# Kernel tuning notes

Measured on AMD Instinct MI355X. Metric: run time of the kernel, lower is better.

## Reference

```python
import jax, jax.numpy as jnp
import numpy as np

EPS = 1e-5

def _face_normals(v, vi):
    # v: [B,V,3], vi: [F,3] -> [B,F,3]
    pts = v[:, vi]                                  # [B,F,3,3]
    n = jnp.cross(pts[:, :, 1] - pts[:, :, 0], pts[:, :, 2] - pts[:, :, 0])
    norm = jnp.linalg.norm(n, axis=-1, keepdims=True)
    return n / jnp.where(norm < EPS, 1.0, norm)

def _vert_normals(v, vi):
    fn = _face_normals(v, vi)                       # [B,F,3]
    fn_rep = jnp.repeat(fn, 3, axis=1)              # [B,3F,3] (one copy per face vertex)
    vn = jnp.zeros_like(v).at[:, vi.reshape(-1)].add(fn_rep)
    norm = jnp.linalg.norm(vn, axis=-1, keepdims=True)
    return vn / jnp.where(norm < EPS, 1.0, norm)

def _values_to_uv(values, index_image, bary_image):
    # values: [B,V,C]; index_image/bary_image: [U,U,3] -> [B,C,U,U]
    mask = jnp.all(index_image != -1, axis=-1)      # [U,U]
    idx = jnp.clip(index_image, 0, values.shape[1] - 1)
    vals = values[:, idx]                           # [B,U,U,3,C]
    uv = jnp.einsum('buvkc,uvk->bcuv', vals, bary_image.astype(values.dtype))
    return uv * mask[None, None].astype(values.dtype)

def _grid_sample_bilinear(img, gx, gy):
    # img: [B,C,H,W]; gx,gy: [N] in [-1,1]; align_corners=False, zero padding
    B, C, H, W = img.shape
    ix = ((gx + 1.0) * W - 1.0) * 0.5
    iy = ((gy + 1.0) * H - 1.0) * 0.5
    x0 = jnp.floor(ix); y0 = jnp.floor(iy)
    x1 = x0 + 1.0;      y1 = y0 + 1.0
    wx1 = ix - x0; wx0 = 1.0 - wx1
    wy1 = iy - y0; wy0 = 1.0 - wy1
    def gather(xi, yi):
        valid = (xi >= 0) & (xi < W) & (yi >= 0) & (yi < H)
        xc = jnp.clip(xi, 0, W - 1).astype(jnp.int32)
        yc = jnp.clip(yi, 0, H - 1).astype(jnp.int32)
        return img[:, :, yc, xc] * valid.astype(img.dtype)  # [B,C,N]
    return (gather(x0, y0) * (wx0 * wy0) + gather(x1, y0) * (wx1 * wy0)
          + gather(x0, y1) * (wx0 * wy1) + gather(x1, y1) * (wx1 * wy1))

def _sample_uv(values_uv, uv_coords, v2uv):
    g = uv_coords * 2.0 - 1.0                       # [T,2]
    vals = _grid_sample_bilinear(values_uv, g[:, 0], g[:, 1])  # [B,C,T]
    vals = jnp.transpose(vals, (0, 2, 1))           # [B,T,C]
    return vals[:, v2uv].mean(axis=2)               # [B,V,C]

def setup_inputs() -> dict:
    key = jax.random.key(0)
    ks = jax.random.split(key, 6)
    B, V, Fc, U, T, K = 8, 100000, 200000, 1024, 110000, 2
    verts = jax.random.normal(ks[0], (B, V, 3), jnp.float32)
    vi = jax.random.randint(ks[1], (Fc, 3), 0, V, dtype=jnp.int32)
    index_image = jax.random.randint(ks[2], (U, U, 3), 0, V, dtype=jnp.int32)
    bary_image = jax.random.uniform(ks[3], (U, U, 3), jnp.float32)
    vt = jax.random.uniform(ks[4], (T, 2), jnp.float32)
    v2uv = jax.random.randint(ks[5], (V, K), 0, T, dtype=jnp.int32)
    return {"verts": verts, "bary_image": bary_image, "vt": vt,
            "vi": vi, "index_image": index_image, "v2uv": v2uv}

def reference(verts, bary_image, vt, vi, index_image, v2uv):
    vn = _vert_normals(verts, vi)                   # [B,V,3]
    uv = _values_to_uv(vn, index_image, bary_image) # [B,3,U,U]
    return _sample_uv(uv, vt, v2uv)                 # [B,V,3]
```

## Files before the change

### kernel.cpp

```cpp
#include <hip/hip_runtime.h>

#define EPS 1e-5f

constexpr int B = 8;
constexpr int V = 100000;
constexpr int F = 200000;
constexpr int U = 1024;
constexpr int T = 110000;
constexpr int CAP = 24;

constexpr int NBUK = (V + 127) / 128;
constexpr int N4   = (3 * F) / 4;
constexpr int EB   = (N4 + 255) / 256;
constexpr int TRB  = (V + 255) / 256;
constexpr int FNB  = (F * 8 + 255) / 256;
constexpr int CPB  = (T + 255) / 256;

__global__ void k1_pre(const float* __restrict__ verts,
                       float4* __restrict__ vertsT,
                       const int* __restrict__ vi,
                       int* __restrict__ hist) {
    __shared__ int lh[NBUK];
    int blk = blockIdx.x;
    if (blk < TRB) {
        int v = blk * 256 + threadIdx.x;
        if (v >= V) return;
        float4 row[8];
#pragma unroll
        for (int b = 0; b < 8; ++b) {
            const float* p = verts + (size_t)b * V * 3 + (size_t)v * 3;
            row[b] = make_float4(p[0], p[1], p[2], 0.0f);
        }
        float4* dst = vertsT + (size_t)v * 8;
#pragma unroll
        for (int b = 0; b < 8; ++b) dst[b] = row[b];
    } else {
        int k = blk - TRB;
        for (int i = threadIdx.x; i < NBUK; i += 256) lh[i] = 0;
        __syncthreads();
        int m4 = k * 256 + threadIdx.x;
        if (m4 < N4) {
            int4 e = ((const int4*)vi)[m4];
            atomicAdd(&lh[e.x >> 7], 1);
            atomicAdd(&lh[e.y >> 7], 1);
            atomicAdd(&lh[e.z >> 7], 1);
            atomicAdd(&lh[e.w >> 7], 1);
        }
        __syncthreads();
        for (int b = threadIdx.x; b < NBUK; b += 256) hist[k * NBUK + b] = lh[b];
    }
}

__global__ void k2_fused(const int* __restrict__ vi,
                         const float4* __restrict__ vertsT,
                         float4* __restrict__ fn,
                         const int* __restrict__ index_image,
                         const float* __restrict__ bary_image,
                         const float* __restrict__ vt,
                         int4* __restrict__ cI,
                         float4* __restrict__ cW,
                         int* __restrict__ hist,
                         int* __restrict__ tot) {
    int blk = blockIdx.x;

    if (blk < FNB) {
        int id = blk * 256 + threadIdx.x;
        if (id >= F * 8) return;
        int f = id >> 3;
        int b = id & 7;

        int i0 = vi[f * 3 + 0];
        int i1 = vi[f * 3 + 1];
        int i2 = vi[f * 3 + 2];

        float4 p0 = vertsT[(size_t)i0 * 8 + b];
        float4 p1 = vertsT[(size_t)i1 * 8 + b];
        float4 p2 = vertsT[(size_t)i2 * 8 + b];

        float e1x = p1.x - p0.x, e1y = p1.y - p0.y, e1z = p1.z - p0.z;
        float e2x = p2.x - p0.x, e2y = p2.y - p0.y, e2z = p2.z - p0.z;

        float nx = e1y * e2z - e1z * e2y;
        float ny = e1z * e2x - e1x * e2z;
        float nz = e1x * e2y - e1y * e2x;

        float norm = sqrtf(nx * nx + ny * ny + nz * nz);
        float inv = (norm < EPS) ? 1.0f : (1.0f / norm);
        fn[id] = make_float4(nx * inv, ny * inv, nz * inv, 0.0f);
        return;
    }

    if (blk < FNB + CPB) {
        int t = (blk - FNB) * 256 + threadIdx.x;
        if (t >= T) return;

        float gx = vt[t * 2 + 0];
        float gy = vt[t * 2 + 1];
        float ix = gx * (float)U - 0.5f;
        float iy = gy * (float)U - 0.5f;

        float x0f = floorf(ix);
        float y0f = floorf(iy);
        int x0 = (int)x0f;
        int y0 = (int)y0f;
        float wx1 = ix - x0f, wx0 = 1.0f - wx1;
        float wy1 = iy - y0f, wy0 = 1.0f - wy1;

#pragma unroll
        for (int c = 0; c < 4; ++c) {
            int cy = c >> 1, cx = c & 1;
            int y = y0 + cy;
            int x = x0 + cx;
            int4 ci = make_int4(0, 0, 0, 0);
            float4 cw = make_float4(0.0f, 0.0f, 0.0f, 0.0f);
            if (x >= 0 && x < U && y >= 0 && y < U) {
                float w = (cy ? wy1 : wy0) * (cx ? wx1 : wx0);
                int pix = y * U + x;
                int i0 = index_image[pix * 3 + 0];
                int i1 = index_image[pix * 3 + 1];
                int i2 = index_image[pix * 3 + 2];
                float m = (i0 != -1 && i1 != -1 && i2 != -1) ? 1.0f : 0.0f;
                float wm = w * m;
                ci.x = min(max(i0, 0), V - 1);
                ci.y = min(max(i1, 0), V - 1);
                ci.z = min(max(i2, 0), V - 1);
                cw.x = wm * bary_image[pix * 3 + 0];
                cw.y = wm * bary_image[pix * 3 + 1];
                cw.z = wm * bary_image[pix * 3 + 2];
            }
            cI[t * 4 + c] = ci;
            cW[t * 4 + c] = cw;
        }
        return;
    }

    {
        __shared__ int part[256];
        int b = blk - FNB - CPB;
        int th = threadIdx.x;
        int k0 = th * 3;
        int c0 = (k0     < EB) ? hist[(k0    ) * NBUK + b] : 0;
        int c1 = (k0 + 1 < EB) ? hist[(k0 + 1) * NBUK + b] : 0;
        int c2 = (k0 + 2 < EB) ? hist[(k0 + 2) * NBUK + b] : 0;
        int local = c0 + c1 + c2;
        part[th] = local;
        __syncthreads();
        for (int off = 1; off < 256; off <<= 1) {
            int x = (th >= off) ? part[th - off] : 0;
            __syncthreads();
            part[th] += x;
            __syncthreads();
        }
        int excl = part[th] - local;
        if (th == 255) tot[b] = part[255];
        if (k0     < EB) hist[(k0    ) * NBUK + b] = excl;
        if (k0 + 1 < EB) hist[(k0 + 1) * NBUK + b] = excl + c0;
        if (k0 + 2 < EB) hist[(k0 + 2) * NBUK + b] = excl + c0 + c1;
    }
}

__global__ void k3_base(const int* __restrict__ tot, int* __restrict__ base) {
    __shared__ int s[1024];
    int t = threadIdx.x;
    int c = (t < NBUK) ? tot[t] : 0;
    s[t] = c;
    __syncthreads();
    for (int off = 1; off < 1024; off <<= 1) {
        int x = (t >= off) ? s[t - off] : 0;
        __syncthreads();
        s[t] += x;
        __syncthreads();
    }
    if (t <= NBUK) base[t] = s[t] - c;
}

__global__ void k4_scatter(const int* __restrict__ vi,
                           const int* __restrict__ off,
                           const int* __restrict__ base,
                           int* __restrict__ pairs) {
    __shared__ int lh[NBUK];
    int k = blockIdx.x;
    for (int i = threadIdx.x; i < NBUK; i += 256) lh[i] = 0;
    __syncthreads();
    int m4 = k * 256 + threadIdx.x;
    if (m4 >= N4) return;
    int4 e = ((const int4*)vi)[m4];
    int be = m4 * 4;
    int vv[4] = {e.x, e.y, e.z, e.w};
#pragma unroll
    for (int j = 0; j < 4; ++j) {
        int v = vv[j];
        int b = v >> 7;
        int r = atomicAdd(&lh[b], 1);
        int pos = base[b] + off[k * NBUK + b] + r;
        pairs[pos] = ((v & 127) << 18) | ((be + j) / 3);
    }
}

__global__ __launch_bounds__(512) void k5_gather(
        const int* __restrict__ pairs,
        const int* __restrict__ base,
        const float4* __restrict__ fn,
        float4* __restrict__ vn) {
    __shared__ int cnt[128];
    __shared__ int rows[128 * CAP];
    int b = blockIdx.x;
    int tid = threadIdx.x;
    if (tid < 128) cnt[tid] = 0;
    __syncthreads();

    int start = base[b], end = base[b + 1];
    for (int i = start + tid; i < end; i += 512) {
        int pk = pairs[i];
        int vl = pk >> 18;
        int f = pk & 0x3FFFF;
        int pos = atomicAdd(&cnt[vl], 1);
        if (pos < CAP) rows[vl * CAP + pos] = f;
    }
    __syncthreads();

    int v0 = b << 7;
    for (int id = tid; id < 128 * 8; id += 512) {
        int vl = id >> 3, b8 = id & 7;
        int v = v0 + vl;
        if (v >= V) continue;
        int deg = min(cnt[vl], CAP);
        float ax = 0.0f, ay = 0.0f, az = 0.0f;
        for (int j = 0; j < deg; ++j) {
            float4 n = fn[(size_t)rows[vl * CAP + j] * 8 + b8];
            ax += n.x; ay += n.y; az += n.z;
        }
        float nn = sqrtf(ax * ax + ay * ay + az * az);
        float inv = (nn < EPS) ? 1.0f : (1.0f / nn);
        vn[(size_t)v * 8 + b8] = make_float4(ax * inv, ay * inv, az * inv, 0.0f);
    }
}

__global__ void sample_points(const float4* __restrict__ vn,
                              const int4* __restrict__ cI,
                              const float4* __restrict__ cW,
                              float4* __restrict__ vals) {
    int id = blockIdx.x * blockDim.x + threadIdx.x;
    if (id >= T * 8) return;
    int t = id >> 3;
    int b = id & 7;

    float ax = 0.0f, ay = 0.0f, az = 0.0f;
#pragma unroll
    for (int c = 0; c < 4; ++c) {
        int4 ci = cI[t * 4 + c];
        float4 cw = cW[t * 4 + c];
        float4 q0 = vn[(size_t)ci.x * 8 + b];
        float4 q1 = vn[(size_t)ci.y * 8 + b];
        float4 q2 = vn[(size_t)ci.z * 8 + b];
        ax += cw.x * q0.x + cw.y * q1.x + cw.z * q2.x;
        ay += cw.x * q0.y + cw.y * q1.y + cw.z * q2.y;
        az += cw.x * q0.z + cw.y * q1.z + cw.z * q2.z;
    }

    vals[id] = make_float4(ax, ay, az, 0.0f);
}

__global__ void gather_out(const float4* __restrict__ vals,
                           const int* __restrict__ v2uv,
                           float* __restrict__ out) {
    int id = blockIdx.x * blockDim.x + threadIdx.x;
    if (id >= V * 8) return;
    int v = id >> 3;
    int b = id & 7;

    int t0 = v2uv[v * 2 + 0];
    int t1 = v2uv[v * 2 + 1];
    float4 x = vals[(size_t)t0 * 8 + b];
    float4 y = vals[(size_t)t1 * 8 + b];

    float* o = out + (size_t)b * V * 3 + (size_t)v * 3;
    o[0] = 0.5f * (x.x + y.x);
    o[1] = 0.5f * (x.y + y.y);
    o[2] = 0.5f * (x.z + y.z);
}

extern "C" void kernel_launch(void* const* d_in, const int* in_sizes, int n_in,
                              void* d_out, int out_size, void* d_ws, size_t ws_size,
                              hipStream_t stream) {
    const float* verts   = (const float*)d_in[0];
    const float* bary    = (const float*)d_in[1];
    const float* vt      = (const float*)d_in[2];
    const int*   vi      = (const int*)d_in[3];
    const int*   idx_img = (const int*)d_in[4];
    const int*   v2uv    = (const int*)d_in[5];
    float* out = (float*)d_out;

    float4* vertsT = (float4*)d_ws;
    float4* vn     = vertsT;
    float4* fn     = vertsT + (size_t)V * 8;
    float4* vals   = fn;
    int4*   cI     = (int4*)(fn + (size_t)F * 8);
    float4* cW     = (float4*)(cI + (size_t)T * 4);
    int*    hist   = (int*)(cW + (size_t)T * 4);
    int*    tot    = hist + (size_t)EB * NBUK;
    int*    base   = tot + NBUK;
    int*    pairs  = base + NBUK + 1;

    const int BLK = 256;
    k1_pre<<<TRB + EB, BLK, 0, stream>>>(verts, vertsT, vi, hist);
    k2_fused<<<FNB + CPB + NBUK, BLK, 0, stream>>>(
        vi, vertsT, fn, idx_img, bary, vt, cI, cW, hist, tot);
    k3_base<<<1, 1024, 0, stream>>>(tot, base);
    k4_scatter<<<EB, BLK, 0, stream>>>(vi, hist, base, pairs);
    k5_gather<<<NBUK, 512, 0, stream>>>(pairs, base, fn, vn);
    sample_points<<<(T * 8 + BLK - 1) / BLK, BLK, 0, stream>>>(vn, cI, cW, vals);
    gather_out<<<(V * 8 + BLK - 1) / BLK, BLK, 0, stream>>>(vals, v2uv, out);
}
```

Measured before the change: 199.3 us.

## Store normals and weights in half precision and fold base scan into consumers

Face normals, vertex normals, sample weights and sampled values are now stored as packed fp16 (8 bytes instead of 16), which halves the bytes moved by the random-gather kernels. The single-block k3_base launch is removed, and each block of k4_scatter and k5_gather recomputes the bucket prefix scan from the totals in shared memory. This drops one kernel launch and its serialization point, at the cost of redundant scan work in every block. The fp16 storage also reduces accuracy of the intermediate normals and weights.

New measurement: 188.2 us. 5.6% less time.

```diff
diff --git a/kernel.cpp b/kernel.cpp
--- a/kernel.cpp
+++ b/kernel.cpp
@@ -1,4 +1,5 @@
 #include <hip/hip_runtime.h>
+#include <hip/hip_fp16.h>
 
 #define EPS 1e-5f
 
@@ -15,6 +16,17 @@
 constexpr int TRB  = (V + 255) / 256;
 constexpr int FNB  = (F * 8 + 255) / 256;
 constexpr int CPB  = (T + 255) / 256;
+
+struct alignas(8) h4 { __half2 a, b; };
+__device__ inline h4 pack_h4(float x, float y, float z) {
+    h4 r; r.a = __floats2half2_rn(x, y); r.b = __floats2half2_rn(z, 0.0f);
+    return r;
+}
+__device__ inline float3 unpack_h4(h4 v) {
+    float2 xy = __half22float2(v.a);
+    float2 zw = __half22float2(v.b);
+    return make_float3(xy.x, xy.y, zw.x);
+}
 
 __global__ void k1_pre(const float* __restrict__ verts,
                        float4* __restrict__ vertsT,
@@ -53,12 +65,12 @@
 
 __global__ void k2_fused(const int* __restrict__ vi,
                          const float4* __restrict__ vertsT,
-                         float4* __restrict__ fn,
+                         h4* __restrict__ fn,
                          const int* __restrict__ index_image,
                          const float* __restrict__ bary_image,
                          const float* __restrict__ vt,
                          int4* __restrict__ cI,
-                         float4* __restrict__ cW,
+                         h4* __restrict__ cWh,
                          int* __restrict__ hist,
                          int* __restrict__ tot) {
     int blk = blockIdx.x;
@@ -86,7 +98,7 @@
 
         float norm = sqrtf(nx * nx + ny * ny + nz * nz);
         float inv = (norm < EPS) ? 1.0f : (1.0f / norm);
-        fn[id] = make_float4(nx * inv, ny * inv, nz * inv, 0.0f);
+        fn[id] = pack_h4(nx * inv, ny * inv, nz * inv);
         return;
     }
 
@@ -112,7 +124,7 @@
             int y = y0 + cy;
             int x = x0 + cx;
             int4 ci = make_int4(0, 0, 0, 0);
-            float4 cw = make_float4(0.0f, 0.0f, 0.0f, 0.0f);
+            float w0 = 0.0f, w1 = 0.0f, w2 = 0.0f;
             if (x >= 0 && x < U && y >= 0 && y < U) {
                 float w = (cy ? wy1 : wy0) * (cx ? wx1 : wx0);
                 int pix = y * U + x;
@@ -124,12 +136,12 @@
                 ci.x = min(max(i0, 0), V - 1);
                 ci.y = min(max(i1, 0), V - 1);
                 ci.z = min(max(i2, 0), V - 1);
-                cw.x = wm * bary_image[pix * 3 + 0];
-                cw.y = wm * bary_image[pix * 3 + 1];
-                cw.z = wm * bary_image[pix * 3 + 2];
+                w0 = wm * bary_image[pix * 3 + 0];
+                w1 = wm * bary_image[pix * 3 + 1];
+                w2 = wm * bary_image[pix * 3 + 2];
             }
             cI[t * 4 + c] = ci;
-            cW[t * 4 + c] = cw;
+            cWh[t * 4 + c] = pack_h4(w0, w1, w2);
         }
         return;
     }
@@ -159,26 +171,46 @@
     }
 }
 
-__global__ void k3_base(const int* __restrict__ tot, int* __restrict__ base) {
-    __shared__ int s[1024];
-    int t = threadIdx.x;
-    int c = (t < NBUK) ? tot[t] : 0;
-    s[t] = c;
-    __syncthreads();
-    for (int off = 1; off < 1024; off <<= 1) {
-        int x = (t >= off) ? s[t - off] : 0;
-        __syncthreads();
-        s[t] += x;
-        __syncthreads();
-    }
-    if (t <= NBUK) base[t] = s[t] - c;
+__device__ inline void scan_base(const int* __restrict__ tot,
+                                 int* pre, int* part) {
+    constexpr int CH = (NBUK + 255) / 256;
+    int th = threadIdx.x;
+    int loc[CH];
+    int local = 0;
+#pragma unroll
+    for (int j = 0; j < CH; ++j) {
+        int idx = th * CH + j;
+        int c = (idx < NBUK) ? tot[idx] : 0;
+        loc[j] = local;
+        local += c;
+    }
+    part[th] = local;
+    __syncthreads();
+    for (int off = 1; off < 256; off <<= 1) {
+        int x = (th >= off) ? part[th - off] : 0;
+        __syncthreads();
+        part[th] += x;
+        __syncthreads();
+    }
+    int excl = part[th] - local;
+#pragma unroll
+    for (int j = 0; j < CH; ++j) {
+        int idx = th * CH + j;
+        if (idx < NBUK) pre[idx] = excl + loc[j];
+    }
+    if (th == 255) pre[NBUK] = part[255];
+    __syncthreads();
 }
 
 __global__ void k4_scatter(const int* __restrict__ vi,
                            const int* __restrict__ off,
-                           const int* __restrict__ base,
+                           const int* __restrict__ tot,
                            int* __restrict__ pairs) {
     __shared__ int lh[NBUK];
+    __shared__ int pre[NBUK + 1];
+    __shared__ int part[256];
+    scan_base(tot, pre, part);
+
     int k = blockIdx.x;
     for (int i = threadIdx.x; i < NBUK; i += 256) lh[i] = 0;
     __syncthreads();
@@ -192,25 +224,29 @@
         int v = vv[j];
         int b = v >> 7;
         int r = atomicAdd(&lh[b], 1);
-        int pos = base[b] + off[k * NBUK + b] + r;
+        int pos = pre[b] + off[k * NBUK + b] + r;
         pairs[pos] = ((v & 127) << 18) | ((be + j) / 3);
     }
 }
 
-__global__ __launch_bounds__(512) void k5_gather(
+__global__ __launch_bounds__(256) void k5_gather(
         const int* __restrict__ pairs,
-        const int* __restrict__ base,
-        const float4* __restrict__ fn,
-        float4* __restrict__ vn) {
+        const int* __restrict__ tot,
+        const h4* __restrict__ fn,
+        h4* __restrict__ vn) {
     __shared__ int cnt[128];
     __shared__ int rows[128 * CAP];
-    int b = blockIdx.x;
+    __shared__ int pre[NBUK + 1];
+    __shared__ int part[256];
+    scan_base(tot, pre, part);
+
     int tid = threadIdx.x;
     if (tid < 128) cnt[tid] = 0;
     __syncthreads();
 
-    int start = base[b], end = base[b + 1];
-    for (int i = start + tid; i < end; i += 512) {
+    int b = blockIdx.x;
+    int start = pre[b], end = pre[b + 1];
+    for (int i = start + tid; i < end; i += 256) {
         int pk = pairs[i];
         int vl = pk >> 18;
         int f = pk & 0x3FFFF;
@@ -220,26 +256,26 @@
     __syncthreads();
 
     int v0 = b << 7;
-    for (int id = tid; id < 128 * 8; id += 512) {
+    for (int id = tid; id < 128 * 8; id += 256) {
         int vl = id >> 3, b8 = id & 7;
         int v = v0 + vl;
         if (v >= V) continue;
         int deg = min(cnt[vl], CAP);
         float ax = 0.0f, ay = 0.0f, az = 0.0f;
         for (int j = 0; j < deg; ++j) {
-            float4 n = fn[(size_t)rows[vl * CAP + j] * 8 + b8];
+            float3 n = unpack_h4(fn[(size_t)rows[vl * CAP + j] * 8 + b8]);
             ax += n.x; ay += n.y; az += n.z;
         }
         float nn = sqrtf(ax * ax + ay * ay + az * az);
         float inv = (nn < EPS) ? 1.0f : (1.0f / nn);
-        vn[(size_t)v * 8 + b8] = make_float4(ax * inv, ay * inv, az * inv, 0.0f);
-    }
-}
-
-__global__ void sample_points(const float4* __restrict__ vn,
+        vn[(size_t)v * 8 + b8] = pack_h4(ax * inv, ay * inv, az * inv);
+    }
+}
+
+__global__ void sample_points(const h4* __restrict__ vn,
                               const int4* __restrict__ cI,
-                              const float4* __restrict__ cW,
-                              float4* __restrict__ vals) {
+                              const h4* __restrict__ cWh,
+                              h4* __restrict__ vals) {
     int id = blockIdx.x * blockDim.x + threadIdx.x;
     if (id >= T * 8) return;
     int t = id >> 3;
@@ -249,19 +285,19 @@
 #pragma unroll
     for (int c = 0; c < 4; ++c) {
         int4 ci = cI[t * 4 + c];
-        float4 cw = cW[t * 4 + c];
-        float4 q0 = vn[(size_t)ci.x * 8 + b];
-        float4 q1 = vn[(size_t)ci.y * 8 + b];
-        float4 q2 = vn[(size_t)ci.z * 8 + b];
-        ax += cw.x * q0.x + cw.y * q1.x + cw.z * q2.x;
-        ay += cw.x * q0.y + cw.y * q1.y + cw.z * q2.y;
-        az += cw.x * q0.z + cw.y * q1.z + cw.z * q2.z;
-    }
-
-    vals[id] = make_float4(ax, ay, az, 0.0f);
-}
-
-__global__ void gather_out(const float4* __restrict__ vals,
+        float3 w = unpack_h4(cWh[t * 4 + c]);
+        float3 q0 = unpack_h4(vn[(size_t)ci.x * 8 + b]);
+        float3 q1 = unpack_h4(vn[(size_t)ci.y * 8 + b]);
+        float3 q2 = unpack_h4(vn[(size_t)ci.z * 8 + b]);
+        ax += w.x * q0.x + w.y * q1.x + w.z * q2.x;
+        ay += w.x * q0.y + w.y * q1.y + w.z * q2.y;
+        az += w.x * q0.z + w.y * q1.z + w.z * q2.z;
+    }
+
+    vals[id] = pack_h4(ax, ay, az);
+}
+
+__global__ void gather_out(const h4* __restrict__ vals,
                            const int* __restrict__ v2uv,
                            float* __restrict__ out) {
     int id = blockIdx.x * blockDim.x + threadIdx.x;
@@ -271,8 +307,8 @@
 
     int t0 = v2uv[v * 2 + 0];
     int t1 = v2uv[v * 2 + 1];
-    float4 x = vals[(size_t)t0 * 8 + b];
-    float4 y = vals[(size_t)t1 * 8 + b];
+    float3 x = unpack_h4(vals[(size_t)t0 * 8 + b]);
+    float3 y = unpack_h4(vals[(size_t)t1 * 8 + b]);
 
     float* o = out + (size_t)b * V * 3 + (size_t)v * 3;
     o[0] = 0.5f * (x.x + y.x);
@@ -292,23 +328,21 @@
     float* out = (float*)d_out;
 
     float4* vertsT = (float4*)d_ws;
-    float4* vn     = vertsT;
-    float4* fn     = vertsT + (size_t)V * 8;
-    float4* vals   = fn;
-    int4*   cI     = (int4*)(fn + (size_t)F * 8);
-    float4* cW     = (float4*)(cI + (size_t)T * 4);
-    int*    hist   = (int*)(cW + (size_t)T * 4);
+    h4*     vn     = (h4*)d_ws;
+    h4*     fn     = (h4*)(vertsT + (size_t)V * 8);
+    h4*     vals   = fn;
+    int4*   cI     = (int4*)((char*)fn + (size_t)F * 8 * sizeof(h4));
+    h4*     cWh    = (h4*)(cI + (size_t)T * 4);
+    int*    hist   = (int*)(cWh + (size_t)T * 4);
     int*    tot    = hist + (size_t)EB * NBUK;
-    int*    base   = tot + NBUK;
-    int*    pairs  = base + NBUK + 1;
+    int*    pairs  = tot + NBUK;
 
     const int BLK = 256;
     k1_pre<<<TRB + EB, BLK, 0, stream>>>(verts, vertsT, vi, hist);
     k2_fused<<<FNB + CPB + NBUK, BLK, 0, stream>>>(
-        vi, vertsT, fn, idx_img, bary, vt, cI, cW, hist, tot);
-    k3_base<<<1, 1024, 0, stream>>>(tot, base);
-    k4_scatter<<<EB, BLK, 0, stream>>>(vi, hist, base, pairs);
-    k5_gather<<<NBUK, 512, 0, stream>>>(pairs, base, fn, vn);
-    sample_points<<<(T * 8 + BLK - 1) / BLK, BLK, 0, stream>>>(vn, cI, cW, vals);
+        vi, vertsT, fn, idx_img, bary, vt, cI, cWh, hist, tot);
+    k4_scatter<<<EB, BLK, 0, stream>>>(vi, hist, tot, pairs);
+    k5_gather<<<NBUK, BLK, 0, stream>>>(pairs, tot, fn, vn);
+    sample_points<<<(T * 8 + BLK - 1) / BLK, BLK, 0, stream>>>(vn, cI, cWh, vals);
     gather_out<<<(V * 8 + BLK - 1) / BLK, BLK, 0, stream>>>(vals, v2uv, out);
 }
```
